# Kernel optimization log

Measured on AMD Instinct MI355X. Metric: run time of the kernel, lower is better.

Reference implementation:

```python
import jax, jax.numpy as jnp
import numpy as np

B, D, N, K, V = 32, 256, 2048, 512, 6
COMMIT = 1.0

def setup_inputs() -> dict:
    key = jax.random.key(0)
    k1, k2 = jax.random.split(key)
    inputs = jax.random.normal(k1, (B, D, N), dtype=jnp.float32)
    embeddings = jax.random.normal(k2, (V, D, K), dtype=jnp.float32)
    return {"inputs": inputs, "embeddings": embeddings}

def _vq_layer(residual, emb):
    # residual: (B, D, N); emb: (D, K) codebook
    flat = residual.transpose(0, 2, 1).reshape(-1, D)                # (B*N, D)
    dist = (jnp.sum(flat * flat, axis=1, keepdims=True)
            + jnp.sum(emb * emb, axis=0, keepdims=True)
            - 2.0 * (flat @ emb))                                    # (B*N, K)
    idx = jnp.argmin(dist, axis=1)                                   # (B*N,)
    q = jnp.take(emb.T, idx, axis=0)                                 # (B*N, D) gather
    q = q.reshape(B, N, D).transpose(0, 2, 1)                        # (B, D, N)
    # straight-through estimator
    q_st = residual + jax.lax.stop_gradient(q - residual)
    loss = COMMIT * jnp.mean(jnp.square(jax.lax.stop_gradient(q) - residual))
    return q_st, idx.reshape(B, N), loss

def reference(inputs, embeddings):
    residual = inputs
    q_sum = jnp.zeros_like(inputs)
    tokens = []
    total_loss = jnp.float32(0.0)
    for v in range(V):  # fixed small layer stack
        q, idx, loss = _vq_layer(residual, embeddings[v])
        q_sum = q_sum + q
        tokens.append(idx)
        total_loss = total_loss + loss
        residual = residual - q
    return q_sum, jnp.stack(tokens, axis=0), total_loss
```

## Files before the change

kernel.cpp:

```cpp
#include <hip/hip_runtime.h>
#include <cfloat>

#define B_  32
#define D_  256
#define N_  2048
#define K_  512
#define V_  6
#define DN_ (D_*N_)
#define DK_ (D_*K_)
#define QSZ (B_*D_*N_)
#define TOKSZ (B_*N_)
#define TOK_OFF QSZ
#define LOSS_OFF (QSZ + V_*TOKSZ)
#define MARGIN 0.02f
#define FCAP 32768
#define TPB 128
#define NBLK (TOKSZ/TPB)

typedef __attribute__((ext_vector_type(8))) short short8b;
typedef __attribute__((ext_vector_type(4))) float f32x4;

__device__ __forceinline__ unsigned short f2bf(float x) {
  unsigned u = __float_as_uint(x);
  unsigned r = (u + 0x7fffu + ((u >> 16) & 1u)) >> 16;
  return (unsigned short)r;
}
__device__ __forceinline__ float bf2f(unsigned short h) {
  return __uint_as_float(((unsigned)h) << 16);
}
__device__ __forceinline__ unsigned orderf(float f) {
  unsigned u = __float_as_uint(f);
  return (u >> 31) ? ~u : (u | 0x80000000u);
}
__device__ __forceinline__ float unorderf(unsigned u) {
  return __uint_as_float((u & 0x80000000u) ? (u & 0x7fffffffu) : ~u);
}
__device__ __forceinline__ unsigned long long shfl_xor_u64(unsigned long long v, int m) {
  int lo = __shfl_xor((int)(unsigned)(v & 0xffffffffull), m, 64);
  int hi = __shfl_xor((int)(unsigned)(v >> 32), m, 64);
  return ((unsigned long long)(unsigned)hi << 32) | (unsigned)lo;
}

__global__ __launch_bounds__(256) void pack_kernel(const float* __restrict__ emb,
                                                   float* __restrict__ Ef32,
                                                   unsigned short* __restrict__ Ehi,
                                                   unsigned short* __restrict__ Elo) {
  __shared__ float T[64][68];
  const int tid = threadIdx.x;
  const int k0 = blockIdx.x * 64, d0 = blockIdx.y * 64, v = blockIdx.z;
  const float* src = emb + (size_t)v * DK_;
  const int r = tid >> 4, c4 = (tid & 15) * 4;
  #pragma unroll
  for (int i = 0; i < 4; ++i) {
    int d = d0 + r + i * 16;
    float4 x = *(const float4*)(src + (size_t)d * K_ + k0 + c4);
    *(float4*)&T[r + i * 16][c4] = x;
  }
  __syncthreads();
  #pragma unroll
  for (int i = 0; i < 4; ++i) {
    int k = k0 + r + i * 16;
    float4 wv;
    wv.x = T[c4 + 0][r + i * 16];
    wv.y = T[c4 + 1][r + i * 16];
    wv.z = T[c4 + 2][r + i * 16];
    wv.w = T[c4 + 3][r + i * 16];
    size_t o = ((size_t)v * K_ + k) * 256 + d0 + c4;
    *(float4*)(Ef32 + o) = wv;
    ushort4 hv, lv;
    hv.x = f2bf(wv.x); lv.x = f2bf(wv.x - bf2f(hv.x));
    hv.y = f2bf(wv.y); lv.y = f2bf(wv.y - bf2f(hv.y));
    hv.z = f2bf(wv.z); lv.z = f2bf(wv.z - bf2f(hv.z));
    hv.w = f2bf(wv.w); lv.w = f2bf(wv.w - bf2f(hv.w));
    *(ushort4*)(Ehi + o) = hv;
    *(ushort4*)(Elo + o) = lv;
  }
}

__global__ __launch_bounds__(256) void en2_kernel(const float* __restrict__ Ef32,
                                                  float* __restrict__ en2f,
                                                  double* __restrict__ en2d) {
  __shared__ double P[64][4];
  const int tid = threadIdx.x;
  const int k = blockIdx.x * 64 + (tid >> 2), q = tid & 3;
  const float* e = Ef32 + (size_t)k * 256 + q * 64;
  double s = 0.0;
  #pragma unroll 8
  for (int i = 0; i < 64; ++i) { double x = (double)e[i]; s = fma(x, x, s); }
  P[tid >> 2][q] = s;
  __syncthreads();
  if (tid < 64) {
    int k2 = blockIdx.x * 64 + tid;
    double t = (P[tid][0] + P[tid][1]) + (P[tid][2] + P[tid][3]);
    en2d[k2] = t;
    en2f[k2] = (float)t;
  }
}

__global__ __launch_bounds__(512) void rvq_fused(
    const float* __restrict__ inputs,
    const unsigned short* __restrict__ Ehi, const unsigned short* __restrict__ Elo,
    const float* __restrict__ Ef32, const float* __restrict__ en2f,
    float* __restrict__ tokens, float* __restrict__ lossPart,
    int* __restrict__ flagCnt, int* __restrict__ flagList)
{
  __shared__ unsigned short Ahi[8 * 4 * TPB * 8];
  __shared__ unsigned short Alo[8 * 4 * TPB * 8];
  __shared__ unsigned long long wmin[8][TPB];
  __shared__ float wsec[8][TPB];
  __shared__ int sIdx[TPB];
  __shared__ float wred[8];

  const int tid = threadIdx.x;
  const int lane = tid & 63, w = tid >> 6;
  const int l15 = lane & 15, lg = lane >> 4;
  const int gt0 = blockIdx.x * TPB;
  const int b = gt0 >> 11, n0 = gt0 & (N_ - 1);
  const int kb = w * 64;

  {
    const int tok = tid & (TPB - 1), cq = tid >> 7;
    const float* src = inputs + (size_t)b * DN_ + n0 + tok;
    #pragma unroll
    for (int cc = 0; cc < 2; ++cc) {
      const int c = cq + cc * 4;
      #pragma unroll
      for (int g = 0; g < 4; ++g) {
        short8b hv, lv;
        #pragma unroll
        for (int e = 0; e < 8; ++e) {
          float x = src[(size_t)(c * 32 + g * 8 + e) * N_];
          unsigned short h = f2bf(x);
          hv[e] = (short)h;
          lv[e] = (short)f2bf(x - bf2f(h));
        }
        *(short8b*)&Ahi[((c * 4 + g) * TPB + tok) * 8] = hv;
        *(short8b*)&Alo[((c * 4 + g) * TPB + tok) * 8] = lv;
      }
    }
  }
  __syncthreads();

  for (int v = 0; v < V_; ++v) {
    const unsigned short* ehiL = Ehi + (size_t)v * DK_ + (size_t)(kb + l15) * 256 + lg * 8;
    const unsigned short* eloL = Elo + (size_t)v * DK_ + (size_t)(kb + l15) * 256 + lg * 8;
    const float* Ef32v = Ef32 + (size_t)v * DK_;

    f32x4 acc[8][4];
    #pragma unroll
    for (int tt = 0; tt < 8; ++tt)
      #pragma unroll
      for (int kt = 0; kt < 4; ++kt) acc[tt][kt] = (f32x4){0.f, 0.f, 0.f, 0.f};

    #pragma unroll
    for (int c = 0; c < 8; ++c) {
      short8b ah[8], al[8];
      #pragma unroll
      for (int tt = 0; tt < 8; ++tt) {
        ah[tt] = *(const short8b*)&Ahi[((c * 4 + lg) * TPB + tt * 16 + l15) * 8];
        al[tt] = *(const short8b*)&Alo[((c * 4 + lg) * TPB + tt * 16 + l15) * 8];
      }
      #pragma unroll
      for (int kt = 0; kt < 4; ++kt) {
        short8b bh = *(const short8b*)(ehiL + (size_t)kt * 4096 + c * 32);
        short8b bl = *(const short8b*)(eloL + (size_t)kt * 4096 + c * 32);
        #pragma unroll
        for (int tt = 0; tt < 8; ++tt) {
          acc[tt][kt] = __builtin_amdgcn_mfma_f32_16x16x32_bf16(ah[tt], bh, acc[tt][kt], 0, 0, 0);
          acc[tt][kt] = __builtin_amdgcn_mfma_f32_16x16x32_bf16(ah[tt], bl, acc[tt][kt], 0, 0, 0);
          acc[tt][kt] = __builtin_amdgcn_mfma_f32_16x16x32_bf16(al[tt], bh, acc[tt][kt], 0, 0, 0);
        }
      }
    }

    float en4[4];
    #pragma unroll
    for (int kt = 0; kt < 4; ++kt) en4[kt] = en2f[v * K_ + kb + kt * 16 + l15];

    #pragma unroll
    for (int tt = 0; tt < 8; ++tt)
      #pragma unroll
      for (int r = 0; r < 4; ++r) {
        const int token = tt * 16 + lg * 4 + r;
        float dv0 = en4[0] - 2.f * acc[tt][0][r];
        unsigned long long p = ((unsigned long long)orderf(dv0) << 32) | (unsigned)(kb + l15);
        float s = FLT_MAX;
        #pragma unroll
        for (int kt = 1; kt < 4; ++kt) {
          float dv = en4[kt] - 2.f * acc[tt][kt][r];
          unsigned long long pk = ((unsigned long long)orderf(dv) << 32) |
                                  (unsigned)(kb + kt * 16 + l15);
          if (pk < p) { s = fminf(s, unorderf((unsigned)(p >> 32))); p = pk; }
          else s = fminf(s, dv);
        }
        #pragma unroll
        for (int m = 1; m <= 8; m <<= 1) {
          unsigned long long po = shfl_xor_u64(p, m);
          float so = __shfl_xor(s, m, 64);
          unsigned long long pmax = (po < p) ? p : po;
          s = fminf(fminf(s, so), unorderf((unsigned)(pmax >> 32)));
          p = (po < p) ? po : p;
        }
        if (l15 == 0) { wmin[w][token] = p; wsec[w][token] = s; }
      }
    __syncthreads();
    if (tid < TPB) {
      unsigned long long p = wmin[0][tid]; float s = wsec[0][tid];
      #pragma unroll
      for (int w2 = 1; w2 < 8; ++w2) {
        unsigned long long po = wmin[w2][tid]; float so = wsec[w2][tid];
        unsigned long long pmax = (po < p) ? p : po;
        s = fminf(fminf(s, so), unorderf((unsigned)(pmax >> 32)));
        p = (po < p) ? po : p;
      }
      int kwin = (int)(p & 0xffffffffull);
      sIdx[tid] = kwin;
      tokens[(size_t)v * TOKSZ + gt0 + tid] = (float)kwin;
      float bd = unorderf((unsigned)(p >> 32));
      if (s - bd < MARGIN) {
        int pos = atomicAdd(flagCnt, 1);
        if (pos < FCAP) flagList[pos] = gt0 + tid;
      }
    }
    __syncthreads();

    const int uj = tid & (TPB - 1), cq = tid >> 7;
    const int kw = sIdx[uj];
    float lacc = 0.f;
    #pragma unroll
    for (int cc = 0; cc < 2; ++cc) {
      const int c = cq * 2 + cc;
      const float* er = Ef32v + (size_t)kw * 256 + c * 32;
      #pragma unroll
      for (int g = 0; g < 4; ++g) {
        unsigned short* ph = &Ahi[((c * 4 + g) * TPB + uj) * 8];
        unsigned short* pl = &Alo[((c * 4 + g) * TPB + uj) * 8];
        short8b h8 = *(const short8b*)ph;
        short8b l8 = *(const short8b*)pl;
        float4 e0 = *(const float4*)(er + g * 8);
        float4 e1 = *(const float4*)(er + g * 8 + 4);
        float ee[8] = {e0.x, e0.y, e0.z, e0.w, e1.x, e1.y, e1.z, e1.w};
        short8b nh, nl;
        #pragma unroll
        for (int jj = 0; jj < 8; ++jj) {
          float rv = bf2f((unsigned short)h8[jj]) + bf2f((unsigned short)l8[jj]);
          float rn = rv - ee[jj];
          unsigned short hh = f2bf(rn);
          nh[jj] = (short)hh;
          nl[jj] = (short)f2bf(rn - bf2f(hh));
          lacc += rn * rn;
        }
        if (v < V_ - 1) {
          *(short8b*)ph = nh;
          *(short8b*)pl = nl;
        }
      }
    }
    #pragma unroll
    for (int m = 32; m >= 1; m >>= 1) lacc += __shfl_xor(lacc, m, 64);
    if (lane == 0) wred[w] = lacc;
    __syncthreads();
    if (tid == 0) {
      float t = 0.f;
      #pragma unroll
      for (int w2 = 0; w2 < 8; ++w2) t += wred[w2];
      lossPart[(size_t)v * NBLK + blockIdx.x] = t;
    }
    __syncthreads();
  }
}

__global__ __launch_bounds__(256) void chain_fixup(
    const float* __restrict__ inputs, const float* __restrict__ Ef32,
    const double* __restrict__ en2d, float* __restrict__ tokens,
    const int* __restrict__ flagList, const int* __restrict__ flagCnt)
{
  __shared__ double rD[256];
  __shared__ double sbd[256];
  __shared__ int sbk[256];
  const int tid = threadIdx.x;
  int cnt = flagCnt[0]; if (cnt > FCAP) cnt = FCAP;
  for (int i = blockIdx.x; i < cnt; i += gridDim.x) {
    const int gt = flagList[i];
    const int b = gt >> 11, n = gt & (N_ - 1);
    rD[tid] = (double)inputs[(size_t)b * DN_ + (size_t)tid * N_ + n];
    __syncthreads();
    for (int v = 0; v < V_; ++v) {
      const float* Ev = Ef32 + (size_t)v * DK_;
      double best = 1.0e300; int bk = 0;
      #pragma unroll
      for (int half = 0; half < 2; ++half) {
        const int k = tid + half * 256;
        const float* e0 = Ev + (size_t)k * 256;
        double s0 = 0.0, s1 = 0.0, s2 = 0.0, s3 = 0.0;
        #pragma unroll 8
        for (int dd = 0; dd < 256; dd += 4) {
          s0 = fma(rD[dd + 0], (double)e0[dd + 0], s0);
          s1 = fma(rD[dd + 1], (double)e0[dd + 1], s1);
          s2 = fma(rD[dd + 2], (double)e0[dd + 2], s2);
          s3 = fma(rD[dd + 3], (double)e0[dd + 3], s3);
        }
        double dist = en2d[v * K_ + k] - 2.0 * ((s0 + s1) + (s2 + s3));
        if (dist < best) { best = dist; bk = k; }
      }
      sbd[tid] = best; sbk[tid] = bk;
      __syncthreads();
      for (int st = 128; st >= 1; st >>= 1) {
        if (tid < st) {
          double od = sbd[tid + st]; int ok = sbk[tid + st];
          if (od < sbd[tid] || (od == sbd[tid] && ok < sbk[tid])) {
            sbd[tid] = od; sbk[tid] = ok;
          }
        }
        __syncthreads();
      }
      const int nk = sbk[0];
      if (tid == 0) tokens[(size_t)v * TOKSZ + gt] = (float)nk;
      double e = (double)Ev[(size_t)nk * 256 + tid];
      __syncthreads();
      rD[tid] = rD[tid] - e;
      __syncthreads();
    }
  }
}

__global__ __launch_bounds__(256) void finalize_q(const float* __restrict__ toks,
                                                  const float* __restrict__ Ef32,
                                                  float* __restrict__ out) {
  const int tid = threadIdx.x;
  const int gt = blockIdx.x * 64 + (tid >> 2);
  const int q = tid & 3;
  const int b = gt >> 11, n = gt & (N_ - 1);
  float4 a[16];
  int k0 = (int)toks[gt];
  const float* e0 = Ef32 + (size_t)k0 * 256 + q * 64;
  #pragma unroll
  for (int i = 0; i < 16; ++i) a[i] = ((const float4*)e0)[i];
  #pragma unroll
  for (int v = 1; v < V_; ++v) {
    int kv = (int)toks[v * TOKSZ + gt];
    const float* ev = Ef32 + (size_t)v * DK_ + (size_t)kv * 256 + q * 64;
    #pragma unroll
    for (int i = 0; i < 16; ++i) {
      float4 e = ((const float4*)ev)[i];
      a[i].x += e.x; a[i].y += e.y; a[i].z += e.z; a[i].w += e.w;
    }
  }
  float* dst = out + (size_t)b * DN_ + n;
  #pragma unroll
  for (int i = 0; i < 16; ++i) {
    int d = q * 64 + i * 4;
    dst[(size_t)(d + 0) * N_] = a[i].x;
    dst[(size_t)(d + 1) * N_] = a[i].y;
    dst[(size_t)(d + 2) * N_] = a[i].z;
    dst[(size_t)(d + 3) * N_] = a[i].w;
  }
}

__global__ __launch_bounds__(256) void loss_kernel(const float* __restrict__ part,
                                                   float* __restrict__ out) {
  __shared__ float s[256];
  const int tid = threadIdx.x;
  float a = 0.f;
  for (int i = tid; i < V_ * NBLK; i += 256) a += part[i];
  s[tid] = a;
  __syncthreads();
  for (int st = 128; st >= 1; st >>= 1) {
    if (tid < st) s[tid] += s[tid + st];
    __syncthreads();
  }
  if (tid == 0) out[LOSS_OFF] = s[0] * (1.0f / (float)QSZ);
}

extern "C" void kernel_launch(void* const* d_in, const int* in_sizes, int n_in,
                              void* d_out, int out_size, void* d_ws, size_t ws_size,
                              hipStream_t stream) {
  (void)in_sizes; (void)n_in; (void)out_size; (void)ws_size;
  const float* inputs = (const float*)d_in[0];
  const float* emb    = (const float*)d_in[1];
  float* out = (float*)d_out;
  char* ws = (char*)d_ws;

  unsigned short* Ehi = (unsigned short*)(ws + 0);
  unsigned short* Elo = (unsigned short*)(ws + 1572864);
  float*  Ef32 = (float*)(ws + 3145728);
  float*  en2f = (float*)(ws + 6291456);
  double* en2d = (double*)(ws + 6303744);
  float*  part = (float*)(ws + 6328320);
  int*    flagCnt  = (int*)(ws + 6340608);
  int*    flagList = (int*)(ws + 6340612);

  float* toks = out + TOK_OFF;

  hipMemsetAsync(flagCnt, 0, sizeof(int), stream);
  pack_kernel<<<dim3(8, 4, 6), 256, 0, stream>>>(emb, Ef32, Ehi, Elo);
  en2_kernel<<<48, 256, 0, stream>>>(Ef32, en2f, en2d);
  rvq_fused<<<NBLK, 512, 0, stream>>>(inputs, Ehi, Elo, Ef32, en2f,
                                      toks, part, flagCnt, flagList);
  chain_fixup<<<2048, 256, 0, stream>>>(inputs, Ef32, en2d, toks, flagList, flagCnt);
  finalize_q<<<TOKSZ / 64, 256, 0, stream>>>(toks, Ef32, out);
  loss_kernel<<<1, 256, 0, stream>>>(part, out);
}
```

Measured before the change: 766.5 us.

## Reorder MFMA loop, drop block barriers via redundant argmin and per-wave loss

Restructures the MFMA inner loop so the eight B fragments for a chunk are loaded up front and the A fragments are loaded one token tile at a time, which lowers peak register pressure. Every thread now redoes the cross-wave argmin reduction itself, so the sIdx shared buffer and one barrier go away. Loss partials are written per wave to global memory rather than reduced through shared memory, removing another barrier. In exchange the loss kernel sums eight times more partials, and the workspace offsets for the flag counters are moved to make room.

```diff
diff --git a/kernel.cpp b/kernel.cpp
--- a/kernel.cpp
+++ b/kernel.cpp
@@ -108,8 +108,6 @@
   __shared__ unsigned short Alo[8 * 4 * TPB * 8];
   __shared__ unsigned long long wmin[8][TPB];
   __shared__ float wsec[8][TPB];
-  __shared__ int sIdx[TPB];
-  __shared__ float wred[8];
 
   const int tid = threadIdx.x;
   const int lane = tid & 63, w = tid >> 6;
@@ -154,22 +152,32 @@
 
     #pragma unroll
     for (int c = 0; c < 8; ++c) {
-      short8b ah[8], al[8];
+      const unsigned short* bph = ehiL + c * 32;
+      const unsigned short* bpl = eloL + c * 32;
+      short8b bh0 = *(const short8b*)(bph);
+      short8b bh1 = *(const short8b*)(bph + 4096);
+      short8b bh2 = *(const short8b*)(bph + 8192);
+      short8b bh3 = *(const short8b*)(bph + 12288);
+      short8b bl0 = *(const short8b*)(bpl);
+      short8b bl1 = *(const short8b*)(bpl + 4096);
+      short8b bl2 = *(const short8b*)(bpl + 8192);
+      short8b bl3 = *(const short8b*)(bpl + 12288);
       #pragma unroll
       for (int tt = 0; tt < 8; ++tt) {
-        ah[tt] = *(const short8b*)&Ahi[((c * 4 + lg) * TPB + tt * 16 + l15) * 8];
-        al[tt] = *(const short8b*)&Alo[((c * 4 + lg) * TPB + tt * 16 + l15) * 8];
-      }
-      #pragma unroll
-      for (int kt = 0; kt < 4; ++kt) {
-        short8b bh = *(const short8b*)(ehiL + (size_t)kt * 4096 + c * 32);
-        short8b bl = *(const short8b*)(eloL + (size_t)kt * 4096 + c * 32);
-        #pragma unroll
-        for (int tt = 0; tt < 8; ++tt) {
-          acc[tt][kt] = __builtin_amdgcn_mfma_f32_16x16x32_bf16(ah[tt], bh, acc[tt][kt], 0, 0, 0);
-          acc[tt][kt] = __builtin_amdgcn_mfma_f32_16x16x32_bf16(ah[tt], bl, acc[tt][kt], 0, 0, 0);
-          acc[tt][kt] = __builtin_amdgcn_mfma_f32_16x16x32_bf16(al[tt], bh, acc[tt][kt], 0, 0, 0);
-        }
+        short8b ah = *(const short8b*)&Ahi[((c * 4 + lg) * TPB + tt * 16 + l15) * 8];
+        short8b al = *(const short8b*)&Alo[((c * 4 + lg) * TPB + tt * 16 + l15) * 8];
+        acc[tt][0] = __builtin_amdgcn_mfma_f32_16x16x32_bf16(ah, bh0, acc[tt][0], 0, 0, 0);
+        acc[tt][0] = __builtin_amdgcn_mfma_f32_16x16x32_bf16(ah, bl0, acc[tt][0], 0, 0, 0);
+        acc[tt][0] = __builtin_amdgcn_mfma_f32_16x16x32_bf16(al, bh0, acc[tt][0], 0, 0, 0);
+        acc[tt][1] = __builtin_amdgcn_mfma_f32_16x16x32_bf16(ah, bh1, acc[tt][1], 0, 0, 0);
+        acc[tt][1] = __builtin_amdgcn_mfma_f32_16x16x32_bf16(ah, bl1, acc[tt][1], 0, 0, 0);
+        acc[tt][1] = __builtin_amdgcn_mfma_f32_16x16x32_bf16(al, bh1, acc[tt][1], 0, 0, 0);
+        acc[tt][2] = __builtin_amdgcn_mfma_f32_16x16x32_bf16(ah, bh2, acc[tt][2], 0, 0, 0);
+        acc[tt][2] = __builtin_amdgcn_mfma_f32_16x16x32_bf16(ah, bl2, acc[tt][2], 0, 0, 0);
+        acc[tt][2] = __builtin_amdgcn_mfma_f32_16x16x32_bf16(al, bh2, acc[tt][2], 0, 0, 0);
+        acc[tt][3] = __builtin_amdgcn_mfma_f32_16x16x32_bf16(ah, bh3, acc[tt][3], 0, 0, 0);
+        acc[tt][3] = __builtin_amdgcn_mfma_f32_16x16x32_bf16(ah, bl3, acc[tt][3], 0, 0, 0);
+        acc[tt][3] = __builtin_amdgcn_mfma_f32_16x16x32_bf16(al, bh3, acc[tt][3], 0, 0, 0);
       }
     }
 
@@ -204,28 +212,26 @@
         if (l15 == 0) { wmin[w][token] = p; wsec[w][token] = s; }
       }
     __syncthreads();
+
+    const int uj = tid & (TPB - 1), cq = tid >> 7;
+    unsigned long long p = wmin[0][uj]; float s = wsec[0][uj];
+    #pragma unroll
+    for (int w2 = 1; w2 < 8; ++w2) {
+      unsigned long long po = wmin[w2][uj]; float so = wsec[w2][uj];
+      unsigned long long pmax = (po < p) ? p : po;
+      s = fminf(fminf(s, so), unorderf((unsigned)(pmax >> 32)));
+      p = (po < p) ? po : p;
+    }
+    const int kw = (int)(p & 0xffffffffull);
     if (tid < TPB) {
-      unsigned long long p = wmin[0][tid]; float s = wsec[0][tid];
-      #pragma unroll
-      for (int w2 = 1; w2 < 8; ++w2) {
-        unsigned long long po = wmin[w2][tid]; float so = wsec[w2][tid];
-        unsigned long long pmax = (po < p) ? p : po;
-        s = fminf(fminf(s, so), unorderf((unsigned)(pmax >> 32)));
-        p = (po < p) ? po : p;
-      }
-      int kwin = (int)(p & 0xffffffffull);
-      sIdx[tid] = kwin;
-      tokens[(size_t)v * TOKSZ + gt0 + tid] = (float)kwin;
+      tokens[(size_t)v * TOKSZ + gt0 + tid] = (float)kw;
       float bd = unorderf((unsigned)(p >> 32));
       if (s - bd < MARGIN) {
         int pos = atomicAdd(flagCnt, 1);
         if (pos < FCAP) flagList[pos] = gt0 + tid;
       }
     }
-    __syncthreads();
-
-    const int uj = tid & (TPB - 1), cq = tid >> 7;
-    const int kw = sIdx[uj];
+
     float lacc = 0.f;
     #pragma unroll
     for (int cc = 0; cc < 2; ++cc) {
@@ -258,14 +264,8 @@
     }
     #pragma unroll
     for (int m = 32; m >= 1; m >>= 1) lacc += __shfl_xor(lacc, m, 64);
-    if (lane == 0) wred[w] = lacc;
-    __syncthreads();
-    if (tid == 0) {
-      float t = 0.f;
-      #pragma unroll
-      for (int w2 = 0; w2 < 8; ++w2) t += wred[w2];
-      lossPart[(size_t)v * NBLK + blockIdx.x] = t;
-    }
+    if (lane == 0)
+      lossPart[((size_t)v * NBLK + blockIdx.x) * 8 + w] = lacc;
     __syncthreads();
   }
 }
@@ -362,7 +362,7 @@
   __shared__ float s[256];
   const int tid = threadIdx.x;
   float a = 0.f;
-  for (int i = tid; i < V_ * NBLK; i += 256) a += part[i];
+  for (int i = tid; i < V_ * NBLK * 8; i += 256) a += part[i];
   s[tid] = a;
   __syncthreads();
   for (int st = 128; st >= 1; st >>= 1) {
@@ -387,8 +387,8 @@
   float*  en2f = (float*)(ws + 6291456);
   double* en2d = (double*)(ws + 6303744);
   float*  part = (float*)(ws + 6328320);
-  int*    flagCnt  = (int*)(ws + 6340608);
-  int*    flagList = (int*)(ws + 6340612);
+  int*    flagCnt  = (int*)(ws + 6426624);
+  int*    flagList = (int*)(ws + 6426628);
 
   float* toks = out + TOK_OFF;
 
```

Result: faster. 732.1 us (-4.5%).
